# Optimization experiments

Hardware: AMD Instinct MI355X
Metric: run time of the kernel (lower is better)

The kernel has to match this reference:

```python
import jax, jax.numpy as jnp
import numpy as np

B, T_STEPS, H, W = 8192, 512, 64, 64


def setup_inputs() -> dict:
    key = jax.random.key(0)
    k_w, k_g, k_i, k_j, k_a = jax.random.split(key, 5)
    walls = (jax.random.uniform(k_w, (B, H, W)) < 0.3).astype(jnp.float32)
    walls = walls.at[:, 0, :].set(1.0).at[:, H - 1, :].set(1.0)
    walls = walls.at[:, :, 0].set(1.0).at[:, :, W - 1].set(1.0)
    # goals: sparse cells with value 10 (the code checks goals[...] == 10)
    goals = jnp.where(jax.random.uniform(k_g, (B, H, W)) < 0.02, 10.0, 0.0).astype(jnp.float32)
    # start positions strictly interior; clear the wall at each start cell
    i0 = jax.random.randint(k_i, (B,), 1, H - 1)
    j0 = jax.random.randint(k_j, (B,), 1, W - 1)
    walls = walls.at[jnp.arange(B), i0, j0].set(0.0)
    world = jnp.stack([walls, goals], axis=1)  # [B, 2, H, W]
    s0 = jnp.stack([i0, j0], axis=1).astype(jnp.float32)  # [B, 2]
    a = jax.random.randint(k_a, (B, T_STEPS), 0, 5).astype(jnp.int32)  # actions in {0..4}
    return {"s0": s0, "a": a, "world": world, "T": T_STEPS}


def _rollout(s0, a, world, T):
    walls = world[:, 0].reshape(world.shape[0], -1)  # [B, H*W]
    goals = world[:, 1].reshape(world.shape[0], -1)  # [B, H*W]
    Wd = world.shape[3]

    def step(s, a_t):
        # action deltas: 1 -> row-1, 2 -> row+1, 3 -> col-1, 4 -> col+1, 0 -> stay
        dr = jnp.where(a_t == 1, -1.0, jnp.where(a_t == 2, 1.0, 0.0))
        dc = jnp.where(a_t == 3, -1.0, jnp.where(a_t == 4, 1.0, 0.0))
        s_new = s + jnp.stack([dr, dc], axis=1).astype(s.dtype)  # [B, 2]
        idx = (s_new[:, 0].astype(jnp.int32) * Wd + s_new[:, 1].astype(jnp.int32))[:, None]
        g = jnp.take_along_axis(goals, idx, axis=1)[:, 0]
        w = jnp.take_along_axis(walls, idx, axis=1)[:, 0]
        hit_goal = g == 10.0
        hit_wall = jnp.logical_and(jnp.logical_not(hit_goal), w == 1.0)
        r = jnp.where(hit_goal, 1.0, jnp.where(hit_wall, -1.0, -0.01)).astype(jnp.float32)
        s_next = jnp.where(hit_wall[:, None], s, s_new)  # revert move on wall hit
        return s_next, (s_next, r)

    _, (s_traj, r_traj) = jax.lax.scan(step, s0, jnp.swapaxes(a[:, :T], 0, 1))
    s_full = jnp.concatenate([s0[:, None, :], jnp.swapaxes(s_traj, 0, 1)], axis=1)  # [B, T+1, 2]
    r0 = jnp.zeros((s0.shape[0], 1), dtype=jnp.float32)
    r_full = jnp.concatenate([r0, jnp.swapaxes(r_traj, 0, 1)], axis=1)  # [B, T+1]
    return s_full, r_full


def reference(s0, a, world, T):
    return _rollout(s0, a, world, T)
```

## Files before the change

### kernel.cpp

```cpp
#include <hip/hip_runtime.h>
#include <stdint.h>

#define T_STEPS 512
#define CELLS   4096
#define EPB     32
#define WPE     256
#define WPAD    257
#define ASTRIDE 132
#define CHUNK   16
#define NCHUNK  (T_STEPS / CHUNK)
#define KPC     (CHUNK / 4)
#define SSTRIDE 34
#define RSTRIDE 18

__device__ __forceinline__ uint32_t code4(float4 w, float4 g) {
    uint32_t b0 = (g.x == 10.0f) ? 2u : ((w.x == 1.0f) ? 1u : 0u);
    uint32_t b1 = (g.y == 10.0f) ? 2u : ((w.y == 1.0f) ? 1u : 0u);
    uint32_t b2 = (g.z == 10.0f) ? 2u : ((w.z == 1.0f) ? 1u : 0u);
    uint32_t b3 = (g.w == 10.0f) ? 2u : ((w.w == 1.0f) ? 1u : 0u);
    return b0 | (b1 << 2) | (b2 << 4) | (b3 << 6);
}

__global__ __launch_bounds__(64) void pack_kernel(
    const float* __restrict__ world, uint32_t* __restrict__ packed)
{
    const int b = blockIdx.x;
    const int t = threadIdx.x;
    const float* wbase = world + (size_t)b * (2 * CELLS);
    const float* gbase = wbase + CELLS;
    #pragma unroll
    for (int h = 0; h < 4; ++h) {
        const int w  = h * 64 + t;
        const int c0 = w * 16;
        uint32_t word = 0;
        #pragma unroll
        for (int j = 0; j < 4; ++j) {
            float4 wf = *(const float4*)(wbase + c0 + 4 * j);
            float4 gf = *(const float4*)(gbase + c0 + 4 * j);
            word |= code4(wf, gf) << (8 * j);
        }
        packed[(size_t)b * WPE + w] = word;
    }
}

__device__ __forceinline__ int actdelta(int a) {
    return (a == 1) ? -64 : ((a == 2) ? 64 : ((a == 3) ? -1 : ((a == 4) ? 1 : 0)));
}

__global__ __launch_bounds__(128) void rollout_kernel(
    const float* __restrict__ s0,
    const int*   __restrict__ act,
    const uint32_t* __restrict__ packed,
    float* __restrict__ out,
    int B)
{
    __shared__ uint32_t wlds[EPB * WPAD];
    __shared__ uint32_t alds[EPB * ASTRIDE];
    __shared__ float    sbuf[2][EPB * SSTRIDE];
    __shared__ float    rbuf[2][EPB * RSTRIDE];

    const int tid = threadIdx.x;
    const int b0  = blockIdx.x * EPB;

    {
        const uint4* gw = (const uint4*)(packed + (size_t)b0 * WPE);
        #pragma unroll 4
        for (int it = 0; it < 16; ++it) {
            const int idx = it * 128 + tid;
            const uint4 v = gw[idx];
            const int env  = idx >> 6;
            const int base = env * WPAD + (idx & 63) * 4;
            wlds[base]     = v.x;
            wlds[base + 1] = v.y;
            wlds[base + 2] = v.z;
            wlds[base + 3] = v.w;
        }
    }
    if (tid < EPB) wlds[tid * WPAD + WPE] = 0u;
    {
        #pragma unroll 4
        for (int it = 0; it < 32; ++it) {
            const int widx = it * 128 + tid;
            const int env  = widx >> 7;
            const int w    = widx & 127;
            const int4 x = *(const int4*)(act + (size_t)(b0 + env) * T_STEPS + w * 4);
            const uint32_t dw = (uint32_t)(actdelta(x.x) & 255)
                              | ((uint32_t)(actdelta(x.y) & 255) << 8)
                              | ((uint32_t)(actdelta(x.z) & 255) << 16)
                              | ((uint32_t)(actdelta(x.w) & 255) << 24);
            alds[env * ASTRIDE + w] = dw;
        }
    }
    __syncthreads();

    float* const s_base = out;
    float* const r_base = out + (size_t)B * (2 * (T_STEPS + 1));

    if (tid < EPB) {
        const float2 si = *(const float2*)(s0 + 2 * (size_t)(b0 + tid));
        *(float2*)(s_base + (size_t)(b0 + tid) * (2 * (T_STEPS + 1))) = si;
        r_base[(size_t)(b0 + tid) * (T_STEPS + 1)] = 0.0f;
    }

    const int e = tid & (EPB - 1);
    const float2 s = *(const float2*)(s0 + 2 * (size_t)(b0 + e));
    int c = (int)s.y;
    int p = ((int)s.x) * 64 + c;
    const uint32_t* myw = wlds + e * WPAD;
    const uint32_t* myd = alds + e * ASTRIDE;
    const int ft = tid - 64;

    auto waddr = [](int q) -> int {
        const int w = (int)((((unsigned)q) >> 4) & 255u);
        return ((unsigned)(q + CELLS) < 2u * CELLS) ? w : WPE;
    };

    for (int chunk = 0; chunk < NCHUNK; ++chunk) {
        if (tid < 64) {
            float* sb = &sbuf[chunk & 1][e * SSTRIDE];
            float* rb = &rbuf[chunk & 1][e * RSTRIDE];
            const uint4 awv = *(const uint4*)(myd + chunk * 4);
            const uint32_t aws[4] = {awv.x, awv.y, awv.z, awv.w};
            #pragma unroll
            for (int k = 0; k < KPC; ++k) {
                const uint32_t aw = aws[k];
                const int e0 = (int)(aw << 24) >> 24;
                const int e1 = (int)(aw << 16) >> 24;
                const int e2 = (int)(aw << 8) >> 24;
                const int e3 = (int)aw >> 24;
                const int es[4] = {e0, e1, e2, e3};
                #pragma unroll
                for (int jj = 0; jj < 2; ++jj) {
                    const int ls = k * 4 + jj * 2;
                    const int ea = es[2 * jj];
                    const int eb = es[2 * jj + 1];
                    const int dca = ea * (ea & 1);
                    const int dcb = eb * (eb & 1);
                    const int q0  = p + ea;
                    const int q10 = p + eb;
                    const int q11 = q0 + eb;
                    const uint32_t w0  = myw[waddr(q0)];
                    const uint32_t w10 = myw[waddr(q10)];
                    const uint32_t w11 = myw[waddr(q11)];
                    const int l0 = (int)((w0 >> ((q0 & 15) << 1)) & 3);
                    const bool hw0 = (l0 == 1);
                    const float rew0 = (l0 == 2) ? 1.0f : (hw0 ? -1.0f : -0.01f);
                    const int p0 = hw0 ? p : q0;
                    const int c0 = hw0 ? c : c + dca;
                    const uint32_t W1 = hw0 ? w10 : w11;
                    const int q1 = p0 + eb;
                    const int l1 = (int)((W1 >> ((q1 & 15) << 1)) & 3);
                    const bool hw1 = (l1 == 1);
                    const float rew1 = (l1 == 2) ? 1.0f : (hw1 ? -1.0f : -0.01f);
                    p = hw1 ? p0 : q1;
                    c = hw1 ? c0 : c0 + dcb;
                    const int r0i = (p0 - c0) >> 6;
                    const int rfi = (p - c) >> 6;
                    *(float2*)(&sb[2 * ls])     = make_float2((float)r0i, (float)c0);
                    *(float2*)(&sb[2 * ls + 2]) = make_float2((float)rfi, (float)c);
                    *(float2*)(&rb[ls]) = make_float2(rew0, rew1);
                }
            }
        } else if (chunk > 0) {
            const int ch  = chunk - 1;
            const int buf = ch & 1;
            #pragma unroll 4
            for (int ee0 = 0; ee0 < EPB; ee0 += 2) {
                const int ee = ee0 + (ft >> 5);
                const int j  = ft & 31;
                const float v = sbuf[buf][ee * SSTRIDE + j];
                s_base[(size_t)(b0 + ee) * (2 * (T_STEPS + 1)) + ch * 32 + 2 + j] = v;
            }
            #pragma unroll 4
            for (int ee0 = 0; ee0 < EPB; ee0 += 4) {
                const int ee = ee0 + (ft >> 4);
                const int j  = ft & 15;
                const float v = rbuf[buf][ee * RSTRIDE + j];
                r_base[(size_t)(b0 + ee) * (T_STEPS + 1) + ch * 16 + 1 + j] = v;
            }
        }
        __syncthreads();
    }
    if (tid >= 64) {
        const int ch  = NCHUNK - 1;
        const int buf = ch & 1;
        #pragma unroll 4
        for (int ee0 = 0; ee0 < EPB; ee0 += 2) {
            const int ee = ee0 + (ft >> 5);
            const int j  = ft & 31;
            const float v = sbuf[buf][ee * SSTRIDE + j];
            s_base[(size_t)(b0 + ee) * (2 * (T_STEPS + 1)) + ch * 32 + 2 + j] = v;
        }
        #pragma unroll 4
        for (int ee0 = 0; ee0 < EPB; ee0 += 4) {
            const int ee = ee0 + (ft >> 4);
            const int j  = ft & 15;
            const float v = rbuf[buf][ee * RSTRIDE + j];
            r_base[(size_t)(b0 + ee) * (T_STEPS + 1) + ch * 16 + 1 + j] = v;
        }
    }
}

extern "C" void kernel_launch(void* const* d_in, const int* in_sizes, int n_in,
                              void* d_out, int out_size, void* d_ws, size_t ws_size,
                              hipStream_t stream) {
    const float* s0    = (const float*)d_in[0];
    const int*   act   = (const int*)d_in[1];
    const float* world = (const float*)d_in[2];
    float*       out   = (float*)d_out;
    uint32_t*    packed = (uint32_t*)d_ws;

    const int B = in_sizes[0] / 2;

    pack_kernel<<<B, 64, 0, stream>>>(world, packed);
    rollout_kernel<<<B / EPB, 128, 0, stream>>>(s0, act, packed, out, B);
}
```

Before: 429.4 us.

## Speculatively prefetch all 4-step wall/goal outcomes to shorten serial dependency chain

Extends the speculative lookahead from 2 to 4 steps. All 15 reachable cell words for the next four moves are loaded from LDS up front, then the right one is picked with selects as each wall-hit flag resolves. It also replaces the unsigned range-check address function with a clamped index into a padded LDS row that has a zero word at each end. The aim is to take LDS latency off the serial per-step chain, at the cost of more LDS reads and more registers per step.

```diff
diff --git a/kernel.cpp b/kernel.cpp
--- a/kernel.cpp
+++ b/kernel.cpp
@@ -5,11 +5,10 @@
 #define CELLS   4096
 #define EPB     32
 #define WPE     256
-#define WPAD    257
+#define WPAD    258
 #define ASTRIDE 132
 #define CHUNK   16
 #define NCHUNK  (T_STEPS / CHUNK)
-#define KPC     (CHUNK / 4)
 #define SSTRIDE 34
 #define RSTRIDE 18
 
@@ -69,14 +68,15 @@
             const int idx = it * 128 + tid;
             const uint4 v = gw[idx];
             const int env  = idx >> 6;
-            const int base = env * WPAD + (idx & 63) * 4;
+            const int base = env * WPAD + 1 + (idx & 63) * 4;
             wlds[base]     = v.x;
             wlds[base + 1] = v.y;
             wlds[base + 2] = v.z;
             wlds[base + 3] = v.w;
         }
     }
-    if (tid < EPB) wlds[tid * WPAD + WPE] = 0u;
+    if (tid < 2 * EPB)
+        wlds[(tid >> 1) * WPAD + ((tid & 1) ? 257 : 0)] = 0u;
     {
         #pragma unroll 4
         for (int it = 0; it < 32; ++it) {
@@ -110,10 +110,13 @@
     const uint32_t* myd = alds + e * ASTRIDE;
     const int ft = tid - 64;
 
-    auto waddr = [](int q) -> int {
-        const int w = (int)((((unsigned)q) >> 4) & 255u);
-        return ((unsigned)(q + CELLS) < 2u * CELLS) ? w : WPE;
-    };
+#define PROBE(S, W, SH)  do {                                              \
+        const int q_  = p + (S);                                           \
+        int wb_ = (q_ >> 4) + ((q_ >> 31) & 256) + 1;                      \
+        wb_ = min(max(wb_, 0), 257);                                       \
+        (W)  = myw[wb_];                                                   \
+        (SH) = (q_ & 15) << 1;                                             \
+    } while (0)
 
     for (int chunk = 0; chunk < NCHUNK; ++chunk) {
         if (tid < 64) {
@@ -122,44 +125,73 @@
             const uint4 awv = *(const uint4*)(myd + chunk * 4);
             const uint32_t aws[4] = {awv.x, awv.y, awv.z, awv.w};
             #pragma unroll
-            for (int k = 0; k < KPC; ++k) {
+            for (int k = 0; k < 4; ++k) {
                 const uint32_t aw = aws[k];
                 const int e0 = (int)(aw << 24) >> 24;
                 const int e1 = (int)(aw << 16) >> 24;
                 const int e2 = (int)(aw << 8) >> 24;
                 const int e3 = (int)aw >> 24;
-                const int es[4] = {e0, e1, e2, e3};
-                #pragma unroll
-                for (int jj = 0; jj < 2; ++jj) {
-                    const int ls = k * 4 + jj * 2;
-                    const int ea = es[2 * jj];
-                    const int eb = es[2 * jj + 1];
-                    const int dca = ea * (ea & 1);
-                    const int dcb = eb * (eb & 1);
-                    const int q0  = p + ea;
-                    const int q10 = p + eb;
-                    const int q11 = q0 + eb;
-                    const uint32_t w0  = myw[waddr(q0)];
-                    const uint32_t w10 = myw[waddr(q10)];
-                    const uint32_t w11 = myw[waddr(q11)];
-                    const int l0 = (int)((w0 >> ((q0 & 15) << 1)) & 3);
-                    const bool hw0 = (l0 == 1);
-                    const float rew0 = (l0 == 2) ? 1.0f : (hw0 ? -1.0f : -0.01f);
-                    const int p0 = hw0 ? p : q0;
-                    const int c0 = hw0 ? c : c + dca;
-                    const uint32_t W1 = hw0 ? w10 : w11;
-                    const int q1 = p0 + eb;
-                    const int l1 = (int)((W1 >> ((q1 & 15) << 1)) & 3);
-                    const bool hw1 = (l1 == 1);
-                    const float rew1 = (l1 == 2) ? 1.0f : (hw1 ? -1.0f : -0.01f);
-                    p = hw1 ? p0 : q1;
-                    c = hw1 ? c0 : c0 + dcb;
-                    const int r0i = (p0 - c0) >> 6;
-                    const int rfi = (p - c) >> 6;
-                    *(float2*)(&sb[2 * ls])     = make_float2((float)r0i, (float)c0);
-                    *(float2*)(&sb[2 * ls + 2]) = make_float2((float)rfi, (float)c);
-                    *(float2*)(&rb[ls]) = make_float2(rew0, rew1);
-                }
+                const int dc0 = e0 * (e0 & 1), dc1 = e1 * (e1 & 1);
+                const int dc2 = e2 * (e2 & 1), dc3 = e3 * (e3 & 1);
+                const int s01 = e0 + e1;
+                const int s12 = e1 + e2, s02 = e0 + e2, s012 = s01 + e2;
+                const int s23 = e2 + e3, s13 = e1 + e3, s03 = e0 + e3;
+                const int s123 = s12 + e3, s023 = s02 + e3, s013 = s01 + e3;
+                const int s0123 = s012 + e3;
+                uint32_t W0, W1_0, W1_1, W2_00, W2_01, W2_10, W2_11;
+                uint32_t W3_000, W3_001, W3_010, W3_011, W3_100, W3_101, W3_110, W3_111;
+                int h0, h1_0, h1_1, h2_00, h2_01, h2_10, h2_11;
+                int h3_000, h3_001, h3_010, h3_011, h3_100, h3_101, h3_110, h3_111;
+                PROBE(e0,    W0,     h0);
+                PROBE(e1,    W1_0,   h1_0);   PROBE(s01,   W1_1,   h1_1);
+                PROBE(e2,    W2_00,  h2_00);  PROBE(s12,   W2_01,  h2_01);
+                PROBE(s02,   W2_10,  h2_10);  PROBE(s012,  W2_11,  h2_11);
+                PROBE(e3,    W3_000, h3_000); PROBE(s23,   W3_001, h3_001);
+                PROBE(s13,   W3_010, h3_010); PROBE(s123,  W3_011, h3_011);
+                PROBE(s03,   W3_100, h3_100); PROBE(s023,  W3_101, h3_101);
+                PROBE(s013,  W3_110, h3_110); PROBE(s0123, W3_111, h3_111);
+
+                const int ls = k * 4;
+                const int v0 = (int)((W0 >> h0) & 3);
+                const bool tk0 = (v0 != 1);
+                const float rew0 = (v0 == 2) ? 1.0f : (tk0 ? -0.01f : -1.0f);
+                const int m0 = (v0 & 1) - 1;
+                p += e0 & m0;  c += dc0 & m0;
+                *(float2*)(&sb[2 * ls]) = make_float2((float)((p - c) >> 6), (float)c);
+                const uint32_t W1 = tk0 ? W1_1 : W1_0;
+                const int      H1 = tk0 ? h1_1 : h1_0;
+                const int v1 = (int)((W1 >> H1) & 3);
+                const bool tk1 = (v1 != 1);
+                const float rew1 = (v1 == 2) ? 1.0f : (tk1 ? -0.01f : -1.0f);
+                const int m1 = (v1 & 1) - 1;
+                p += e1 & m1;  c += dc1 & m1;
+                *(float2*)(&sb[2 * ls + 2]) = make_float2((float)((p - c) >> 6), (float)c);
+                *(float2*)(&rb[ls]) = make_float2(rew0, rew1);
+                const uint32_t W2 = tk0 ? (tk1 ? W2_11 : W2_10)
+                                        : (tk1 ? W2_01 : W2_00);
+                const int      H2 = tk0 ? (tk1 ? h2_11 : h2_10)
+                                        : (tk1 ? h2_01 : h2_00);
+                const int v2 = (int)((W2 >> H2) & 3);
+                const bool tk2 = (v2 != 1);
+                const float rew2 = (v2 == 2) ? 1.0f : (tk2 ? -0.01f : -1.0f);
+                const int m2 = (v2 & 1) - 1;
+                p += e2 & m2;  c += dc2 & m2;
+                *(float2*)(&sb[2 * ls + 4]) = make_float2((float)((p - c) >> 6), (float)c);
+                const uint32_t W3 = tk0 ? (tk1 ? (tk2 ? W3_111 : W3_110)
+                                               : (tk2 ? W3_101 : W3_100))
+                                        : (tk1 ? (tk2 ? W3_011 : W3_010)
+                                               : (tk2 ? W3_001 : W3_000));
+                const int      H3 = tk0 ? (tk1 ? (tk2 ? h3_111 : h3_110)
+                                               : (tk2 ? h3_101 : h3_100))
+                                        : (tk1 ? (tk2 ? h3_011 : h3_010)
+                                               : (tk2 ? h3_001 : h3_000));
+                const int v3 = (int)((W3 >> H3) & 3);
+                const bool tk3 = (v3 != 1);
+                const float rew3 = (v3 == 2) ? 1.0f : (tk3 ? -0.01f : -1.0f);
+                const int m3 = (v3 & 1) - 1;
+                p += e3 & m3;  c += dc3 & m3;
+                *(float2*)(&sb[2 * ls + 6]) = make_float2((float)((p - c) >> 6), (float)c);
+                *(float2*)(&rb[ls + 2]) = make_float2(rew2, rew3);
             }
         } else if (chunk > 0) {
             const int ch  = chunk - 1;
@@ -199,6 +231,7 @@
             r_base[(size_t)(b0 + ee) * (T_STEPS + 1) + ch * 16 + 1 + j] = v;
         }
     }
+#undef PROBE
 }
 
 extern "C" void kernel_launch(void* const* d_in, const int* in_sizes, int n_in,
```

New measurement: 477.6 us. +11.2%, slower.

## Spread rollout across more waves with per-wave writeback and no block barriers

Applied to the files above, without the earlier changes.

Halves environments per block to 16 and uses 256-thread blocks in which each wavefront simulates 4 environments and writes its own trajectory chunks. This replaces the separate writer warps, the double-buffered staging and the per-chunk __syncthreads. The aim is to put many more latency-bound serial rollout chains in flight per CU and remove barrier stalls. In exchange, lanes within a wave redundantly compute the same environment, and correctness now relies on wave-synchronous LDS reuse of the staging buffers.

```diff
diff --git a/kernel.cpp b/kernel.cpp
--- a/kernel.cpp
+++ b/kernel.cpp
@@ -3,7 +3,8 @@
 
 #define T_STEPS 512
 #define CELLS   4096
-#define EPB     32
+#define EPB     16
+#define EPW     4
 #define WPE     256
 #define WPAD    257
 #define ASTRIDE 132
@@ -47,7 +48,7 @@
     return (a == 1) ? -64 : ((a == 2) ? 64 : ((a == 3) ? -1 : ((a == 4) ? 1 : 0)));
 }
 
-__global__ __launch_bounds__(128) void rollout_kernel(
+__global__ __launch_bounds__(256, 2) void rollout_kernel(
     const float* __restrict__ s0,
     const int*   __restrict__ act,
     const uint32_t* __restrict__ packed,
@@ -56,17 +57,17 @@
 {
     __shared__ uint32_t wlds[EPB * WPAD];
     __shared__ uint32_t alds[EPB * ASTRIDE];
-    __shared__ float    sbuf[2][EPB * SSTRIDE];
-    __shared__ float    rbuf[2][EPB * RSTRIDE];
+    __shared__ float    sbuf[EPB * SSTRIDE];
+    __shared__ float    rbuf[EPB * RSTRIDE];
 
     const int tid = threadIdx.x;
     const int b0  = blockIdx.x * EPB;
 
     {
         const uint4* gw = (const uint4*)(packed + (size_t)b0 * WPE);
-        #pragma unroll 4
-        for (int it = 0; it < 16; ++it) {
-            const int idx = it * 128 + tid;
+        #pragma unroll
+        for (int it = 0; it < 4; ++it) {
+            const int idx = it * 256 + tid;
             const uint4 v = gw[idx];
             const int env  = idx >> 6;
             const int base = env * WPAD + (idx & 63) * 4;
@@ -78,9 +79,9 @@
     }
     if (tid < EPB) wlds[tid * WPAD + WPE] = 0u;
     {
-        #pragma unroll 4
-        for (int it = 0; it < 32; ++it) {
-            const int widx = it * 128 + tid;
+        #pragma unroll
+        for (int it = 0; it < 8; ++it) {
+            const int widx = it * 256 + tid;
             const int env  = widx >> 7;
             const int w    = widx & 127;
             const int4 x = *(const int4*)(act + (size_t)(b0 + env) * T_STEPS + w * 4);
@@ -102,13 +103,16 @@
         r_base[(size_t)(b0 + tid) * (T_STEPS + 1)] = 0.0f;
     }
 
-    const int e = tid & (EPB - 1);
+    const int wv   = tid >> 6;
+    const int lane = tid & 63;
+    const int e    = EPW * wv + (lane & (EPW - 1));
     const float2 s = *(const float2*)(s0 + 2 * (size_t)(b0 + e));
     int c = (int)s.y;
     int p = ((int)s.x) * 64 + c;
     const uint32_t* myw = wlds + e * WPAD;
     const uint32_t* myd = alds + e * ASTRIDE;
-    const int ft = tid - 64;
+    float* sb = &sbuf[e * SSTRIDE];
+    float* rb = &rbuf[e * RSTRIDE];
 
     auto waddr = [](int q) -> int {
         const int w = (int)((((unsigned)q) >> 4) & 255u);
@@ -116,87 +120,60 @@
     };
 
     for (int chunk = 0; chunk < NCHUNK; ++chunk) {
-        if (tid < 64) {
-            float* sb = &sbuf[chunk & 1][e * SSTRIDE];
-            float* rb = &rbuf[chunk & 1][e * RSTRIDE];
-            const uint4 awv = *(const uint4*)(myd + chunk * 4);
-            const uint32_t aws[4] = {awv.x, awv.y, awv.z, awv.w};
+        const uint4 awv = *(const uint4*)(myd + chunk * 4);
+        const uint32_t aws[4] = {awv.x, awv.y, awv.z, awv.w};
+        #pragma unroll
+        for (int k = 0; k < KPC; ++k) {
+            const uint32_t aw = aws[k];
+            const int e0 = (int)(aw << 24) >> 24;
+            const int e1 = (int)(aw << 16) >> 24;
+            const int e2 = (int)(aw << 8) >> 24;
+            const int e3 = (int)aw >> 24;
+            const int es[4] = {e0, e1, e2, e3};
             #pragma unroll
-            for (int k = 0; k < KPC; ++k) {
-                const uint32_t aw = aws[k];
-                const int e0 = (int)(aw << 24) >> 24;
-                const int e1 = (int)(aw << 16) >> 24;
-                const int e2 = (int)(aw << 8) >> 24;
-                const int e3 = (int)aw >> 24;
-                const int es[4] = {e0, e1, e2, e3};
-                #pragma unroll
-                for (int jj = 0; jj < 2; ++jj) {
-                    const int ls = k * 4 + jj * 2;
-                    const int ea = es[2 * jj];
-                    const int eb = es[2 * jj + 1];
-                    const int dca = ea * (ea & 1);
-                    const int dcb = eb * (eb & 1);
-                    const int q0  = p + ea;
-                    const int q10 = p + eb;
-                    const int q11 = q0 + eb;
-                    const uint32_t w0  = myw[waddr(q0)];
-                    const uint32_t w10 = myw[waddr(q10)];
-                    const uint32_t w11 = myw[waddr(q11)];
-                    const int l0 = (int)((w0 >> ((q0 & 15) << 1)) & 3);
-                    const bool hw0 = (l0 == 1);
-                    const float rew0 = (l0 == 2) ? 1.0f : (hw0 ? -1.0f : -0.01f);
-                    const int p0 = hw0 ? p : q0;
-                    const int c0 = hw0 ? c : c + dca;
-                    const uint32_t W1 = hw0 ? w10 : w11;
-                    const int q1 = p0 + eb;
-                    const int l1 = (int)((W1 >> ((q1 & 15) << 1)) & 3);
-                    const bool hw1 = (l1 == 1);
-                    const float rew1 = (l1 == 2) ? 1.0f : (hw1 ? -1.0f : -0.01f);
-                    p = hw1 ? p0 : q1;
-                    c = hw1 ? c0 : c0 + dcb;
-                    const int r0i = (p0 - c0) >> 6;
-                    const int rfi = (p - c) >> 6;
-                    *(float2*)(&sb[2 * ls])     = make_float2((float)r0i, (float)c0);
-                    *(float2*)(&sb[2 * ls + 2]) = make_float2((float)rfi, (float)c);
-                    *(float2*)(&rb[ls]) = make_float2(rew0, rew1);
-                }
-            }
-        } else if (chunk > 0) {
-            const int ch  = chunk - 1;
-            const int buf = ch & 1;
-            #pragma unroll 4
-            for (int ee0 = 0; ee0 < EPB; ee0 += 2) {
-                const int ee = ee0 + (ft >> 5);
-                const int j  = ft & 31;
-                const float v = sbuf[buf][ee * SSTRIDE + j];
-                s_base[(size_t)(b0 + ee) * (2 * (T_STEPS + 1)) + ch * 32 + 2 + j] = v;
-            }
-            #pragma unroll 4
-            for (int ee0 = 0; ee0 < EPB; ee0 += 4) {
-                const int ee = ee0 + (ft >> 4);
-                const int j  = ft & 15;
-                const float v = rbuf[buf][ee * RSTRIDE + j];
-                r_base[(size_t)(b0 + ee) * (T_STEPS + 1) + ch * 16 + 1 + j] = v;
+            for (int jj = 0; jj < 2; ++jj) {
+                const int ls = k * 4 + jj * 2;
+                const int ea = es[2 * jj];
+                const int eb = es[2 * jj + 1];
+                const int dca = ea * (ea & 1);
+                const int dcb = eb * (eb & 1);
+                const int q0  = p + ea;
+                const int q10 = p + eb;
+                const int q11 = q0 + eb;
+                const uint32_t w0  = myw[waddr(q0)];
+                const uint32_t w10 = myw[waddr(q10)];
+                const uint32_t w11 = myw[waddr(q11)];
+                const int l0 = (int)((w0 >> ((q0 & 15) << 1)) & 3);
+                const bool hw0 = (l0 == 1);
+                const float rew0 = (l0 == 2) ? 1.0f : (hw0 ? -1.0f : -0.01f);
+                const int p0 = hw0 ? p : q0;
+                const int c0 = hw0 ? c : c + dca;
+                const uint32_t W1 = hw0 ? w10 : w11;
+                const int q1 = p0 + eb;
+                const int l1 = (int)((W1 >> ((q1 & 15) << 1)) & 3);
+                const bool hw1 = (l1 == 1);
+                const float rew1 = (l1 == 2) ? 1.0f : (hw1 ? -1.0f : -0.01f);
+                p = hw1 ? p0 : q1;
+                c = hw1 ? c0 : c0 + dcb;
+                const int r0i = (p0 - c0) >> 6;
+                const int rfi = (p - c) >> 6;
+                *(float2*)(&sb[2 * ls])     = make_float2((float)r0i, (float)c0);
+                *(float2*)(&sb[2 * ls + 2]) = make_float2((float)rfi, (float)c);
+                *(float2*)(&rb[ls]) = make_float2(rew0, rew1);
             }
         }
-        __syncthreads();
-    }
-    if (tid >= 64) {
-        const int ch  = NCHUNK - 1;
-        const int buf = ch & 1;
-        #pragma unroll 4
-        for (int ee0 = 0; ee0 < EPB; ee0 += 2) {
-            const int ee = ee0 + (ft >> 5);
-            const int j  = ft & 31;
-            const float v = sbuf[buf][ee * SSTRIDE + j];
-            s_base[(size_t)(b0 + ee) * (2 * (T_STEPS + 1)) + ch * 32 + 2 + j] = v;
+        #pragma unroll
+        for (int i = 0; i < 2; ++i) {
+            const int ee = EPW * wv + 2 * i + (lane >> 5);
+            const int j  = lane & 31;
+            const float v = sbuf[ee * SSTRIDE + j];
+            s_base[(size_t)(b0 + ee) * (2 * (T_STEPS + 1)) + chunk * 32 + 2 + j] = v;
         }
-        #pragma unroll 4
-        for (int ee0 = 0; ee0 < EPB; ee0 += 4) {
-            const int ee = ee0 + (ft >> 4);
-            const int j  = ft & 15;
-            const float v = rbuf[buf][ee * RSTRIDE + j];
-            r_base[(size_t)(b0 + ee) * (T_STEPS + 1) + ch * 16 + 1 + j] = v;
+        {
+            const int ee = EPW * wv + (lane >> 4);
+            const int j  = lane & 15;
+            const float v = rbuf[ee * RSTRIDE + j];
+            r_base[(size_t)(b0 + ee) * (T_STEPS + 1) + chunk * 16 + 1 + j] = v;
         }
     }
 }
@@ -213,5 +190,5 @@
     const int B = in_sizes[0] / 2;
 
     pack_kernel<<<B, 64, 0, stream>>>(world, packed);
-    rollout_kernel<<<B / EPB, 128, 0, stream>>>(s0, act, packed, out, B);
+    rollout_kernel<<<B / EPB, 256, 0, stream>>>(s0, act, packed, out, B);
 }
```

Measured after the change: 449.9 us. 4.8% more time.
